# Kernel tuning notes

Measured on AMD Instinct MI355X. Metric: run time of the kernel, lower is better.

The kernel has to match this reference:

```python
import jax, jax.numpy as jnp
import numpy as np

B, WIN, D, H, O, P = 512, 128, 256, 512, 64, 64  # batch, window, input_size, hidden, output, plength


def setup_inputs() -> dict:
    key = jax.random.key(0)
    ks = jax.random.split(key, 14)
    s = 0.05
    return {
        "x": jax.random.normal(ks[0], (B, WIN, D), jnp.float32),
        # AdditiveScore params: V (v_d,), W (v_d, 2H), U (v_d, k_d) with v_d = k_d = D
        "V": jax.random.normal(ks[1], (D,), jnp.float32) * s,
        "W": jax.random.normal(ks[2], (D, 2 * H), jnp.float32) * s,
        "U": jax.random.normal(ks[3], (D, D), jnp.float32) * s,
        # LSTM (1 layer, gate order i,f,g,o): input dim D+O
        "W_ih": jax.random.normal(ks[4], (4 * H, D + O), jnp.float32) * s,
        "W_hh": jax.random.normal(ks[5], (4 * H, H), jnp.float32) * s,
        "b_ih": jax.random.normal(ks[6], (4 * H,), jnp.float32) * s,
        "b_hh": jax.random.normal(ks[7], (4 * H,), jnp.float32) * s,
        # dense: hidden -> output
        "Wd": jax.random.normal(ks[8], (O, H), jnp.float32) * s,
        "bd": jax.random.normal(ks[9], (O,), jnp.float32) * s,
        # context_s / context_c: input -> hidden
        "Ws": jax.random.normal(ks[10], (H, D), jnp.float32) * s,
        "bs": jax.random.normal(ks[11], (H,), jnp.float32) * s,
        "Wc": jax.random.normal(ks[12], (H, D), jnp.float32) * s,
        "bc": jax.random.normal(ks[13], (H,), jnp.float32) * s,
    }


def reference(x, V, W, U, W_ih, W_hh, b_ih, b_hh, Wd, bd, Ws, bs, Wc, bc):
    # initial decoder state from last encoder step
    h0 = jnp.tanh(x[:, -1] @ Ws.T + bs)            # (B, H)
    c0 = jax.nn.sigmoid(x[:, -1] @ Wc.T + bc)      # (B, H)
    y0 = jnp.zeros((x.shape[0], bd.shape[0]), x.dtype)
    # U*k is constant across decode steps: precompute once
    Uk = jnp.einsum('vd,bwd->bvw', U, x)

    def step(carry, _):
        h, c, y = carry
        q = jnp.concatenate([h, c], axis=-1)        # (B, 2H)
        Wq = q @ W.T                                # (B, D)
        # e = V^T tanh(Wq + Uk); softmax over window
        score = jnp.einsum('v,bvw->bw', V, jnp.tanh(Wq[:, :, None] + Uk))
        att = jax.nn.softmax(score, axis=-1)
        ctx = jnp.einsum('bw,bwd->bd', att, x)      # (B, D)
        inp = jnp.concatenate([y, ctx], axis=-1)    # (B, O+D)
        gates = inp @ W_ih.T + h @ W_hh.T + b_ih + b_hh
        i_, f_, g_, o_ = jnp.split(gates, 4, axis=-1)
        c_new = jax.nn.sigmoid(f_) * c + jax.nn.sigmoid(i_) * jnp.tanh(g_)
        h_new = jax.nn.sigmoid(o_) * jnp.tanh(c_new)
        y_new = h_new @ Wd.T + bd                   # (B, O)
        return (h_new, c_new, y_new), (y_new, att)

    _, (ys, atts) = jax.lax.scan(step, (h0, c0, y0), None, length=P)
    predict_y = jnp.transpose(ys, (1, 0, 2))        # (B, P, O)
    weight = jnp.transpose(atts, (1, 0, 2))
    return predict_y, weight
```

## Files before the change

### kernel.cpp

```cpp
#include <hip/hip_runtime.h>
#include <hip/hip_bf16.h>

#define B_   512
#define WIN_ 128
#define D_   256
#define H_   512
#define O_   64
#define P_   64
#define K2H  1024
#define KG   832
#define NQY  320

typedef __attribute__((ext_vector_type(8))) short bf16x8;
typedef __attribute__((ext_vector_type(4))) float f32x4;
using bf16 = __hip_bfloat16;

__device__ __forceinline__ float fast_tanh(float x){
    float e = __expf(2.f * x);
    return 1.f - __fdividef(2.f, e + 1.f);
}
__device__ __forceinline__ float fast_sig(float x){
    return __fdividef(1.f, 1.f + __expf(-x));
}
__device__ __forceinline__ float b_lo(unsigned int u){ return __uint_as_float(u << 16); }
__device__ __forceinline__ float b_hi(unsigned int u){ return __uint_as_float(u & 0xffff0000u); }
__device__ __forceinline__ unsigned int pack2(float a, float b){
    unsigned short sa = __builtin_bit_cast(unsigned short, __float2bfloat16(a));
    unsigned short sb = __builtin_bit_cast(unsigned short, __float2bfloat16(b));
    return (unsigned int)sa | ((unsigned int)sb << 16);
}

__global__ void k_prep(const float* __restrict__ x, const float* __restrict__ W,
                       const float* __restrict__ U, const float* __restrict__ W_ih,
                       const float* __restrict__ W_hh, const float* __restrict__ b_ih,
                       const float* __restrict__ b_hh, const float* __restrict__ Wd,
                       const float* __restrict__ Ws, const float* __restrict__ Wc,
                       bf16* __restrict__ x_bf, bf16* __restrict__ Wcomb,
                       bf16* __restrict__ Wqy, bf16* __restrict__ U_bf,
                       bf16* __restrict__ Wsc, float* __restrict__ bsum,
                       bf16* __restrict__ A0)
{
    const long NX  = (long)B_ * WIN_ * D_;
    const long NWC = (long)2048 * KG;
    const long NWQ = (long)NQY * K2H;
    const long NU  = (long)D_ * D_;
    const long NWS = (long)K2H * D_;
    const long NB  = 2048;
    const long NAY = (long)B_ * O_;
    const long total = NX + NWC + NWQ + NU + NWS + NB + NAY;
    for (long i = (long)blockIdx.x * blockDim.x + threadIdx.x; i < total;
         i += (long)gridDim.x * blockDim.x) {
        long j = i;
        if (j < NX) { x_bf[j] = __float2bfloat16(x[j]); continue; }
        j -= NX;
        if (j < NWC) {
            long n = j / KG, k = j % KG;
            float v = (k < 320) ? W_ih[n * 320 + k] : W_hh[n * 512 + (k - 320)];
            Wcomb[j] = __float2bfloat16(v); continue;
        }
        j -= NWC;
        if (j < NWQ) {
            long n = j / K2H, k = j % K2H;
            float v;
            if (n < 256) v = W[n * K2H + k];
            else { long o = n - 256; v = (k < 512) ? Wd[o * 512 + k] : 0.f; }
            Wqy[j] = __float2bfloat16(v); continue;
        }
        j -= NWQ;
        if (j < NU) { U_bf[j] = __float2bfloat16(U[j]); continue; }
        j -= NU;
        if (j < NWS) {
            long n = j / D_, k = j % D_;
            float v = (n < 512) ? Ws[n * D_ + k] : Wc[(n - 512) * D_ + k];
            Wsc[j] = __float2bfloat16(v); continue;
        }
        j -= NWS;
        if (j < NB) { bsum[j] = b_ih[j] + b_hh[j]; continue; }
        j -= NB;
        { long b = j / O_, o = j % O_; A0[b * KG + o] = __float2bfloat16(0.f); }
    }
}

__global__ void __launch_bounds__(256) k_init2(const bf16* __restrict__ x_bf,
                       const bf16* __restrict__ Wsc, const float* __restrict__ bs,
                       const float* __restrict__ bc, bf16* __restrict__ q_buf,
                       bf16* __restrict__ A0, float* __restrict__ c_f32)
{
    int wave = threadIdx.x >> 6, lane = threadIdx.x & 63;
    int m0 = blockIdx.x * 16;
    int n0 = blockIdx.y * 64 + wave * 16;
    int r = lane & 15, ko = (lane >> 4) * 8, rj = (lane >> 4) * 4;
    const short* xp = (const short*)x_bf;
    const short* wp = (const short*)Wsc;
    f32x4 acc = {};
    #pragma unroll
    for (int k0 = 0; k0 < D_; k0 += 32) {
        bf16x8 a  = *(const bf16x8*)(xp + (long)(m0 + r) * (WIN_ * D_) + 127 * D_ + k0 + ko);
        bf16x8 bb = *(const bf16x8*)(wp + (long)(n0 + r) * D_ + k0 + ko);
        acc = __builtin_amdgcn_mfma_f32_16x16x32_bf16(a, bb, acc, 0, 0, 0);
    }
    int n = n0 + r;
    if (n0 < 512) {
        float bias = bs[n];
        #pragma unroll
        for (int j = 0; j < 4; ++j) {
            int b = m0 + rj + j;
            float hv = fast_tanh(acc[j] + bias);
            bf16 hb = __float2bfloat16(hv);
            q_buf[(long)b * K2H + n]    = hb;
            A0[(long)b * KG + 320 + n]  = hb;
        }
    } else {
        float bias = bc[n - 512];
        #pragma unroll
        for (int j = 0; j < 4; ++j) {
            int b = m0 + rj + j;
            float cv = fast_sig(acc[j] + bias);
            q_buf[(long)b * K2H + n]        = __float2bfloat16(cv);
            c_f32[(long)b * H_ + (n - 512)] = cv;
        }
    }
}

__global__ void __launch_bounds__(256) k_uk(const bf16* __restrict__ U_bf,
                    const bf16* __restrict__ x_bf, bf16* __restrict__ Uk)
{
    __shared__ __align__(16) short xs[64][264];
    int b  = blockIdx.y;
    int v0 = (blockIdx.x >> 1) * 64;
    int w0 = (blockIdx.x & 1) * 64;
    {
        const short* xg = (const short*)x_bf + (long)b * (WIN_ * D_) + (long)w0 * D_;
        int row = threadIdx.x >> 2, cc = (threadIdx.x & 3) * 64;
        #pragma unroll
        for (int i = 0; i < 8; ++i)
            *(bf16x8*)(&xs[row][cc + i * 8]) = *(const bf16x8*)(xg + (long)row * D_ + cc + i * 8);
    }
    __syncthreads();
    int lane = threadIdx.x & 63;
    int wave = threadIdx.x >> 6;
    int r  = lane & 15;
    int ko = (lane >> 4) * 8;
    const short* Up = (const short*)U_bf + (long)(v0 + wave * 16 + r) * D_;
    f32x4 acc[4] = {};
    #pragma unroll 2
    for (int k0 = 0; k0 < D_; k0 += 32) {
        bf16x8 a = *(const bf16x8*)(Up + k0 + ko);
        #pragma unroll
        for (int f = 0; f < 4; ++f) {
            bf16x8 bb = *(const bf16x8*)(&xs[f * 16 + r][k0 + ko]);
            acc[f] = __builtin_amdgcn_mfma_f32_16x16x32_bf16(a, bb, acc[f], 0, 0, 0);
        }
    }
    bf16* up = Uk + (long)b * (D_ * WIN_);
    int vbase = v0 + wave * 16 + (lane >> 4) * 4;
    #pragma unroll
    for (int f = 0; f < 4; ++f) {
        int w = w0 + f * 16 + r;
        #pragma unroll
        for (int j = 0; j < 4; ++j)
            up[(long)(vbase + j) * WIN_ + w] = __float2bfloat16(acc[f][j]);
    }
}

__global__ void __launch_bounds__(64) k_wqy(const bf16* __restrict__ q_buf,
                     const bf16* __restrict__ Wqy, const float* __restrict__ bd,
                     float* __restrict__ Wq, float* __restrict__ out_y,
                     bf16* __restrict__ A_buf, int ystep)
{
    int m0 = blockIdx.x * 16;
    int n0 = blockIdx.y * 32;
    int lane = threadIdx.x & 63;
    int r  = lane & 15;
    int ko = (lane >> 4) * 8;
    const short* qp = (const short*)q_buf;
    const short* wp = (const short*)Wqy;
    f32x4 acc[2] = {};
    for (int k0 = 0; k0 < K2H; k0 += 32) {
        bf16x8 a = *(const bf16x8*)(qp + (long)(m0 + r) * K2H + k0 + ko);
        #pragma unroll
        for (int f = 0; f < 2; ++f) {
            bf16x8 bb = *(const bf16x8*)(wp + (long)(n0 + f*16 + r) * K2H + k0 + ko);
            acc[f] = __builtin_amdgcn_mfma_f32_16x16x32_bf16(a, bb, acc[f], 0, 0, 0);
        }
    }
    #pragma unroll
    for (int f = 0; f < 2; ++f) {
        int n = n0 + f * 16 + r;
        #pragma unroll
        for (int j = 0; j < 4; ++j) {
            int b = m0 + (lane >> 4) * 4 + j;
            float val = acc[f][j];
            if (n < 256) {
                Wq[(long)b * D_ + n] = val;
            } else if (ystep >= 0) {
                int o = n - 256;
                val += bd[o];
                out_y[((long)b * P_ + ystep) * O_ + o] = val;
                A_buf[(long)b * KG + o] = __float2bfloat16(val);
            }
        }
    }
}

__global__ void __launch_bounds__(512) k_att(
    const bf16* __restrict__ x_bf, const bf16* __restrict__ Uk,
    const float* __restrict__ Wq, const float* __restrict__ V,
    bf16* __restrict__ A_cur, float* __restrict__ out_w, int s)
{
    __shared__ float v_s[D_];
    __shared__ float wq_s[2][D_];
    __shared__ float part[2][4][WIN_];
    __shared__ float att_s[2][WIN_];
    __shared__ float cpart[2][2][D_];
    __shared__ float redw[2][4];

    const int tid = threadIdx.x;
    const int b0  = blockIdx.x * 2;
    const int tb  = tid >> 8;
    const int t2  = tid & 255;

    if (tid < D_) v_s[tid] = V[tid];
    { int bb = tid >> 8, n = tid & 255; wq_s[bb][n] = Wq[(long)(b0 + bb) * D_ + n]; }
    __syncthreads();

    const int b = b0 + tb;
    {
        int w2 = t2 & 63, vq = t2 >> 6;
        const unsigned int* ukp =
            (const unsigned int*)(Uk + (long)b * (D_ * WIN_) + (long)vq * 64 * WIN_) + w2;
        float sc0 = 0.f, sc1 = 0.f;
        #pragma unroll 8
        for (int i = 0; i < 64; ++i) {
            unsigned int u = ukp[(long)i * 64];
            int v = vq * 64 + i;
            float wqv = wq_s[tb][v], vv = v_s[v];
            sc0 += vv * fast_tanh(wqv + b_lo(u));
            sc1 += vv * fast_tanh(wqv + b_hi(u));
        }
        part[tb][vq][w2 * 2]     = sc0;
        part[tb][vq][w2 * 2 + 1] = sc1;
    }
    __syncthreads();
    float e = 0.f, scw = 0.f;
    if (t2 < WIN_) {
        scw = part[tb][0][t2] + part[tb][1][t2] + part[tb][2][t2] + part[tb][3][t2];
        float m = scw;
        #pragma unroll
        for (int off = 32; off > 0; off >>= 1) m = fmaxf(m, __shfl_xor(m, off));
        if ((tid & 63) == 0) redw[tb][t2 >> 6] = m;
    }
    __syncthreads();
    if (t2 < WIN_) {
        float m = fmaxf(redw[tb][0], redw[tb][1]);
        e = __expf(scw - m);
        float l = e;
        #pragma unroll
        for (int off = 32; off > 0; off >>= 1) l += __shfl_xor(l, off);
        if ((tid & 63) == 0) redw[tb][2 + (t2 >> 6)] = l;
    }
    __syncthreads();
    if (t2 < WIN_) {
        float l = redw[tb][2] + redw[tb][3];
        float a = __fdividef(e, l);
        att_s[tb][t2] = a;
        out_w[((long)b * P_ + s) * WIN_ + t2] = a;
    }
    __syncthreads();
    {
        int d2 = t2 & 127, wh = t2 >> 7;
        const unsigned int* xp =
            (const unsigned int*)(x_bf + (long)b * (WIN_ * D_) + (long)wh * 64 * D_) + d2;
        float c0 = 0.f, c1 = 0.f;
        #pragma unroll 8
        for (int i = 0; i < 64; ++i) {
            unsigned int u = xp[(long)i * 128];
            float a = att_s[tb][wh * 64 + i];
            c0 += a * b_lo(u);
            c1 += a * b_hi(u);
        }
        cpart[tb][wh][d2 * 2]     = c0;
        cpart[tb][wh][d2 * 2 + 1] = c1;
    }
    __syncthreads();
    if (t2 < 128) {
        int d = t2 * 2;
        float f0 = cpart[tb][0][d] + cpart[tb][1][d];
        float f1 = cpart[tb][0][d + 1] + cpart[tb][1][d + 1];
        *(unsigned int*)(A_cur + (long)b * KG + O_ + d) = pack2(f0, f1);
    }
}

__global__ void __launch_bounds__(256) k_gates(const bf16* __restrict__ A_in,
                     const bf16* __restrict__ Wcomb, const float* __restrict__ bsum,
                     float* __restrict__ c_f32, bf16* __restrict__ A_out,
                     bf16* __restrict__ q_buf)
{
    int m0 = blockIdx.x * 64 + (threadIdx.x >> 6) * 16;
    int j0 = blockIdx.y * 16;
    int lane = threadIdx.x & 63;
    int r  = lane & 15;
    int ko = (lane >> 4) * 8;
    const short* ap = (const short*)A_in;
    const short* wp = (const short*)Wcomb;
    f32x4 acc[4] = {};
    long arow = (long)(m0 + r) * KG;
    #pragma unroll 2
    for (int k0 = 0; k0 < KG; k0 += 32) {
        bf16x8 a = *(const bf16x8*)(ap + arow + k0 + ko);
        #pragma unroll
        for (int g = 0; g < 4; ++g) {
            bf16x8 bb = *(const bf16x8*)(wp + (long)(g * H_ + j0 + r) * KG + k0 + ko);
            acc[g] = __builtin_amdgcn_mfma_f32_16x16x32_bf16(a, bb, acc[g], 0, 0, 0);
        }
    }
    int jj = j0 + r;
    float bi = bsum[jj], bff = bsum[H_ + jj], bg = bsum[2*H_ + jj], bo = bsum[3*H_ + jj];
    int rj = (lane >> 4) * 4;
    #pragma unroll
    for (int j = 0; j < 4; ++j) {
        int b = m0 + rj + j;
        float iv = acc[0][j] + bi;
        float fv = acc[1][j] + bff;
        float gv = acc[2][j] + bg;
        float ov = acc[3][j] + bo;
        float c_old = c_f32[(long)b * H_ + jj];
        float cn = fast_sig(fv) * c_old + fast_sig(iv) * fast_tanh(gv);
        float hn = fast_sig(ov) * fast_tanh(cn);
        c_f32[(long)b * H_ + jj] = cn;
        bf16 hb = __float2bfloat16(hn);
        A_out[(long)b * KG + 320 + jj]  = hb;
        q_buf[(long)b * K2H + jj]       = hb;
        q_buf[(long)b * K2H + H_ + jj]  = __float2bfloat16(cn);
    }
}

__global__ void __launch_bounds__(256) k_yfin(const bf16* __restrict__ q_buf,
                     const bf16* __restrict__ Wqy, const float* __restrict__ bd,
                     float* __restrict__ out_y)
{
    int b = blockIdx.x * 4 + (threadIdx.x >> 6);
    int o = threadIdx.x & 63;
    const short* wdr = (const short*)Wqy + (long)(256 + o) * K2H;
    const short* qh  = (const short*)q_buf + (long)b * K2H;
    float acc = bd[o];
    #pragma unroll 4
    for (int k = 0; k < 512; k += 8) {
        bf16x8 w8 = *(const bf16x8*)(wdr + k);
        bf16x8 h8 = *(const bf16x8*)(qh + k);
        #pragma unroll
        for (int i = 0; i < 8; ++i)
            acc = fmaf(__uint_as_float(((unsigned int)(unsigned short)w8[i]) << 16),
                       __uint_as_float(((unsigned int)(unsigned short)h8[i]) << 16), acc);
    }
    out_y[((long)b * P_ + 63) * O_ + o] = acc;
}

extern "C" void kernel_launch(void* const* d_in, const int* in_sizes, int n_in,
                              void* d_out, int out_size, void* d_ws, size_t ws_size,
                              hipStream_t stream)
{
    const float* x    = (const float*)d_in[0];
    const float* V    = (const float*)d_in[1];
    const float* W    = (const float*)d_in[2];
    const float* U    = (const float*)d_in[3];
    const float* W_ih = (const float*)d_in[4];
    const float* W_hh = (const float*)d_in[5];
    const float* b_ih = (const float*)d_in[6];
    const float* b_hh = (const float*)d_in[7];
    const float* Wd   = (const float*)d_in[8];
    const float* bd   = (const float*)d_in[9];
    const float* Ws   = (const float*)d_in[10];
    const float* bs   = (const float*)d_in[11];
    const float* Wc   = (const float*)d_in[12];
    const float* bc   = (const float*)d_in[13];

    float* out_y = (float*)d_out;
    float* out_w = (float*)d_out + (long)B_ * P_ * O_;

    char* p = (char*)d_ws;
    auto alloc = [&](size_t bytes) { char* r = p; p += (bytes + 255) & ~(size_t)255; return r; };
    bf16*  x_bf  = (bf16*) alloc((size_t)B_ * WIN_ * D_ * 2);
    bf16*  Uk    = (bf16*) alloc((size_t)B_ * D_ * WIN_ * 2);
    bf16*  q_buf = (bf16*) alloc((size_t)B_ * K2H * 2);
    bf16*  A0    = (bf16*) alloc((size_t)B_ * KG * 2);
    bf16*  A1    = (bf16*) alloc((size_t)B_ * KG * 2);
    float* Wq    = (float*)alloc((size_t)B_ * D_ * 4);
    float* c_f32 = (float*)alloc((size_t)B_ * H_ * 4);
    bf16*  Wqy   = (bf16*) alloc((size_t)NQY * K2H * 2);
    bf16*  Wcomb = (bf16*) alloc((size_t)2048 * KG * 2);
    bf16*  U_bf  = (bf16*) alloc((size_t)D_ * D_ * 2);
    bf16*  Wsc   = (bf16*) alloc((size_t)K2H * D_ * 2);
    float* bsum  = (float*)alloc((size_t)2048 * 4);
    bf16*  Abuf[2] = { A0, A1 };

    k_prep<<<4096, 256, 0, stream>>>(x, W, U, W_ih, W_hh, b_ih, b_hh, Wd, Ws, Wc,
                                     x_bf, Wcomb, Wqy, U_bf, Wsc, bsum, A0);
    k_init2<<<dim3(32, 16), 256, 0, stream>>>(x_bf, Wsc, bs, bc, q_buf, A0, c_f32);
    k_uk<<<dim3(8, 512), 256, 0, stream>>>(U_bf, x_bf, Uk);

    for (int s = 0; s < P_; ++s) {
        k_wqy<<<dim3(32, 10), 64, 0, stream>>>(q_buf, Wqy, bd, Wq, out_y,
                                               Abuf[s & 1], s - 1);
        k_att<<<256, 512, 0, stream>>>(x_bf, Uk, Wq, V, Abuf[s & 1], out_w, s);
        k_gates<<<dim3(8, 32), 256, 0, stream>>>(Abuf[s & 1], Wcomb, bsum,
                                                 c_f32, Abuf[(s + 1) & 1], q_buf);
    }
    k_yfin<<<128, 256, 0, stream>>>(q_buf, Wqy, bd, out_y);
}
```

Measured before the change: 2.930 ms.

## Fuse Wq/y projection into gates kernel via split-K partial slabs

Removes the separate per-step k_wqy launch. Each gates block already owns a 64-column slice of h and c, so it computes a split-K partial product of that slice with a sliced W/Wd weight and writes the result to a slab buffer. The attention kernel then sums the 8 partial slabs to form Wq and y. The attention kernel also moves from two batch rows per block to one row per 256-thread block, and x conversion in prep is vectorised. This saves one launch and one q_buf round trip per step, at the cost of extra fp32 slab traffic and an 8-way reduction in k_att.

```diff
diff --git a/kernel.cpp b/kernel.cpp
--- a/kernel.cpp
+++ b/kernel.cpp
@@ -9,7 +9,8 @@
 #define P_   64
 #define K2H  1024
 #define KG   832
-#define NQY  320
+#define NG   2048
+#define NSLN 320
 
 typedef __attribute__((ext_vector_type(8))) short bf16x8;
 typedef __attribute__((ext_vector_type(4))) float f32x4;
@@ -24,6 +25,9 @@
 }
 __device__ __forceinline__ float b_lo(unsigned int u){ return __uint_as_float(u << 16); }
 __device__ __forceinline__ float b_hi(unsigned int u){ return __uint_as_float(u & 0xffff0000u); }
+__device__ __forceinline__ short f2bs(float v){
+    return (short)__builtin_bit_cast(unsigned short, __float2bfloat16(v));
+}
 __device__ __forceinline__ unsigned int pack2(float a, float b){
     unsigned short sa = __builtin_bit_cast(unsigned short, __float2bfloat16(a));
     unsigned short sb = __builtin_bit_cast(unsigned short, __float2bfloat16(b));
@@ -36,37 +40,46 @@
                        const float* __restrict__ b_hh, const float* __restrict__ Wd,
                        const float* __restrict__ Ws, const float* __restrict__ Wc,
                        bf16* __restrict__ x_bf, bf16* __restrict__ Wcomb,
-                       bf16* __restrict__ Wqy, bf16* __restrict__ U_bf,
-                       bf16* __restrict__ Wsc, float* __restrict__ bsum,
-                       bf16* __restrict__ A0)
-{
-    const long NX  = (long)B_ * WIN_ * D_;
-    const long NWC = (long)2048 * KG;
-    const long NWQ = (long)NQY * K2H;
+                       bf16* __restrict__ Wsl, bf16* __restrict__ U_bf,
+                       bf16* __restrict__ Wsc, float* __restrict__ bsum)
+{
+    const long NXv = (long)B_ * WIN_ * D_ / 8;
+    const long NWC = (long)NG * KG;
+    const long NSL = (long)8 * NSLN * 128;
     const long NU  = (long)D_ * D_;
     const long NWS = (long)K2H * D_;
-    const long NB  = 2048;
-    const long NAY = (long)B_ * O_;
-    const long total = NX + NWC + NWQ + NU + NWS + NB + NAY;
+    const long NB  = NG;
+    const long total = NXv + NWC + NSL + NU + NWS + NB;
     for (long i = (long)blockIdx.x * blockDim.x + threadIdx.x; i < total;
          i += (long)gridDim.x * blockDim.x) {
         long j = i;
-        if (j < NX) { x_bf[j] = __float2bfloat16(x[j]); continue; }
-        j -= NX;
+        if (j < NXv) {
+            const float4* xp = (const float4*)x + j * 2;
+            float4 a = xp[0], b = xp[1];
+            bf16x8 v;
+            v[0] = f2bs(a.x); v[1] = f2bs(a.y); v[2] = f2bs(a.z); v[3] = f2bs(a.w);
+            v[4] = f2bs(b.x); v[5] = f2bs(b.y); v[6] = f2bs(b.z); v[7] = f2bs(b.w);
+            *(bf16x8*)((short*)x_bf + j * 8) = v;
+            continue;
+        }
+        j -= NXv;
         if (j < NWC) {
             long n = j / KG, k = j % KG;
             float v = (k < 320) ? W_ih[n * 320 + k] : W_hh[n * 512 + (k - 320)];
             Wcomb[j] = __float2bfloat16(v); continue;
         }
         j -= NWC;
-        if (j < NWQ) {
-            long n = j / K2H, k = j % K2H;
+        if (j < NSL) {
+            long by = j / (NSLN * 128);
+            long rem = j % (NSLN * 128);
+            long n = rem / 128, k = rem % 128;
             float v;
-            if (n < 256) v = W[n * K2H + k];
-            else { long o = n - 256; v = (k < 512) ? Wd[o * 512 + k] : 0.f; }
-            Wqy[j] = __float2bfloat16(v); continue;
-        }
-        j -= NWQ;
+            if (n < 256) v = (k < 64) ? W[n * K2H + by * 64 + k]
+                                      : W[n * K2H + 512 + by * 64 + (k - 64)];
+            else         v = (k < 64) ? Wd[(n - 256) * H_ + by * 64 + k] : 0.f;
+            Wsl[j] = __float2bfloat16(v); continue;
+        }
+        j -= NSL;
         if (j < NU) { U_bf[j] = __float2bfloat16(U[j]); continue; }
         j -= NU;
         if (j < NWS) {
@@ -75,9 +88,7 @@
             Wsc[j] = __float2bfloat16(v); continue;
         }
         j -= NWS;
-        if (j < NB) { bsum[j] = b_ih[j] + b_hh[j]; continue; }
-        j -= NB;
-        { long b = j / O_, o = j % O_; A0[b * KG + o] = __float2bfloat16(0.f); }
+        bsum[j] = b_ih[j] + b_hh[j];
     }
 }
 
@@ -107,8 +118,8 @@
             int b = m0 + rj + j;
             float hv = fast_tanh(acc[j] + bias);
             bf16 hb = __float2bfloat16(hv);
-            q_buf[(long)b * K2H + n]    = hb;
-            A0[(long)b * KG + 320 + n]  = hb;
+            q_buf[(long)b * K2H + n]   = hb;
+            A0[(long)b * KG + 320 + n] = hb;
         }
     } else {
         float bias = bc[n - 512];
@@ -163,70 +174,73 @@
     }
 }
 
-__global__ void __launch_bounds__(64) k_wqy(const bf16* __restrict__ q_buf,
-                     const bf16* __restrict__ Wqy, const float* __restrict__ bd,
-                     float* __restrict__ Wq, float* __restrict__ out_y,
-                     bf16* __restrict__ A_buf, int ystep)
-{
-    int m0 = blockIdx.x * 16;
-    int n0 = blockIdx.y * 32;
-    int lane = threadIdx.x & 63;
-    int r  = lane & 15;
-    int ko = (lane >> 4) * 8;
+__global__ void __launch_bounds__(256) k_slab0(const bf16* __restrict__ q_buf,
+                     const bf16* __restrict__ Wsl, float* __restrict__ slab)
+{
+    int bx = blockIdx.x, by = blockIdx.y;
+    int wave = threadIdx.x >> 6, lane = threadIdx.x & 63;
+    int r = lane & 15, ko = (lane >> 4) * 8, rj = (lane >> 4) * 4;
+    int m0 = bx * 16;
     const short* qp = (const short*)q_buf;
-    const short* wp = (const short*)Wqy;
-    f32x4 acc[2] = {};
-    for (int k0 = 0; k0 < K2H; k0 += 32) {
-        bf16x8 a = *(const bf16x8*)(qp + (long)(m0 + r) * K2H + k0 + ko);
-        #pragma unroll
-        for (int f = 0; f < 2; ++f) {
-            bf16x8 bb = *(const bf16x8*)(wp + (long)(n0 + f*16 + r) * K2H + k0 + ko);
-            acc[f] = __builtin_amdgcn_mfma_f32_16x16x32_bf16(a, bb, acc[f], 0, 0, 0);
-        }
-    }
-    #pragma unroll
-    for (int f = 0; f < 2; ++f) {
-        int n = n0 + f * 16 + r;
-        #pragma unroll
-        for (int j = 0; j < 4; ++j) {
-            int b = m0 + (lane >> 4) * 4 + j;
-            float val = acc[f][j];
-            if (n < 256) {
-                Wq[(long)b * D_ + n] = val;
-            } else if (ystep >= 0) {
-                int o = n - 256;
-                val += bd[o];
-                out_y[((long)b * P_ + ystep) * O_ + o] = val;
-                A_buf[(long)b * KG + o] = __float2bfloat16(val);
-            }
-        }
-    }
-}
-
-__global__ void __launch_bounds__(512) k_att(
+    const short* wp = (const short*)Wsl + (long)by * NSLN * 128;
+    #pragma unroll
+    for (int i = 0; i < 5; ++i) {
+        int n0 = (wave * 5 + i) * 16;
+        f32x4 acc = {};
+        #pragma unroll
+        for (int k0 = 0; k0 < 128; k0 += 32) {
+            long koff = (k0 < 64) ? (by * 64 + k0) : (512 + by * 64 + (k0 - 64));
+            bf16x8 a  = *(const bf16x8*)(qp + (long)(m0 + r) * K2H + koff + ko);
+            bf16x8 bb = *(const bf16x8*)(wp + (long)(n0 + r) * 128 + k0 + ko);
+            acc = __builtin_amdgcn_mfma_f32_16x16x32_bf16(a, bb, acc, 0, 0, 0);
+        }
+        int n = n0 + r;
+        #pragma unroll
+        for (int j = 0; j < 4; ++j)
+            slab[((long)by * B_ + m0 + rj + j) * NSLN + n] = acc[j];
+    }
+}
+
+__global__ void __launch_bounds__(256) k_att(
     const bf16* __restrict__ x_bf, const bf16* __restrict__ Uk,
-    const float* __restrict__ Wq, const float* __restrict__ V,
-    bf16* __restrict__ A_cur, float* __restrict__ out_w, int s)
+    const float* __restrict__ slab, const float* __restrict__ V,
+    const float* __restrict__ bd, bf16* __restrict__ A_cur,
+    float* __restrict__ out_y, float* __restrict__ out_w, int s)
 {
     __shared__ float v_s[D_];
-    __shared__ float wq_s[2][D_];
-    __shared__ float part[2][4][WIN_];
-    __shared__ float att_s[2][WIN_];
-    __shared__ float cpart[2][2][D_];
-    __shared__ float redw[2][4];
-
-    const int tid = threadIdx.x;
-    const int b0  = blockIdx.x * 2;
-    const int tb  = tid >> 8;
-    const int t2  = tid & 255;
-
-    if (tid < D_) v_s[tid] = V[tid];
-    { int bb = tid >> 8, n = tid & 255; wq_s[bb][n] = Wq[(long)(b0 + bb) * D_ + n]; }
-    __syncthreads();
-
-    const int b = b0 + tb;
+    __shared__ float wq_s[D_];
+    __shared__ float part[4][WIN_];
+    __shared__ float att_s[WIN_];
+    __shared__ float cpart[2][D_];
+    __shared__ float redw[4];
+
+    const int b = blockIdx.x;
+    const int t = threadIdx.x;
+
+    v_s[t] = V[t];
     {
-        int w2 = t2 & 63, vq = t2 >> 6;
+        float wsum = 0.f;
+        #pragma unroll
+        for (int by = 0; by < 8; ++by)
+            wsum += slab[((long)by * B_ + b) * NSLN + t];
+        wq_s[t] = wsum;
+    }
+    if (t < O_) {
+        float yv = bd[t];
+        #pragma unroll
+        for (int by = 0; by < 8; ++by)
+            yv += slab[((long)by * B_ + b) * NSLN + 256 + t];
+        if (s > 0) {
+            out_y[((long)b * P_ + (s - 1)) * O_ + t] = yv;
+            A_cur[(long)b * KG + t] = __float2bfloat16(yv);
+        } else {
+            A_cur[(long)b * KG + t] = __float2bfloat16(0.f);
+        }
+    }
+    __syncthreads();
+
+    {
+        int w2 = t & 63, vq = t >> 6;
         const unsigned int* ukp =
             (const unsigned int*)(Uk + (long)b * (D_ * WIN_) + (long)vq * 64 * WIN_) + w2;
         float sc0 = 0.f, sc1 = 0.f;
@@ -234,73 +248,73 @@
         for (int i = 0; i < 64; ++i) {
             unsigned int u = ukp[(long)i * 64];
             int v = vq * 64 + i;
-            float wqv = wq_s[tb][v], vv = v_s[v];
+            float wqv = wq_s[v], vv = v_s[v];
             sc0 += vv * fast_tanh(wqv + b_lo(u));
             sc1 += vv * fast_tanh(wqv + b_hi(u));
         }
-        part[tb][vq][w2 * 2]     = sc0;
-        part[tb][vq][w2 * 2 + 1] = sc1;
+        part[vq][w2 * 2]     = sc0;
+        part[vq][w2 * 2 + 1] = sc1;
     }
     __syncthreads();
     float e = 0.f, scw = 0.f;
-    if (t2 < WIN_) {
-        scw = part[tb][0][t2] + part[tb][1][t2] + part[tb][2][t2] + part[tb][3][t2];
+    if (t < WIN_) {
+        scw = part[0][t] + part[1][t] + part[2][t] + part[3][t];
         float m = scw;
         #pragma unroll
         for (int off = 32; off > 0; off >>= 1) m = fmaxf(m, __shfl_xor(m, off));
-        if ((tid & 63) == 0) redw[tb][t2 >> 6] = m;
-    }
-    __syncthreads();
-    if (t2 < WIN_) {
-        float m = fmaxf(redw[tb][0], redw[tb][1]);
+        if ((t & 63) == 0) redw[t >> 6] = m;
+    }
+    __syncthreads();
+    if (t < WIN_) {
+        float m = fmaxf(redw[0], redw[1]);
         e = __expf(scw - m);
         float l = e;
         #pragma unroll
         for (int off = 32; off > 0; off >>= 1) l += __shfl_xor(l, off);
-        if ((tid & 63) == 0) redw[tb][2 + (t2 >> 6)] = l;
-    }
-    __syncthreads();
-    if (t2 < WIN_) {
-        float l = redw[tb][2] + redw[tb][3];
-        float a = __fdividef(e, l);
-        att_s[tb][t2] = a;
-        out_w[((long)b * P_ + s) * WIN_ + t2] = a;
+        if ((t & 63) == 0) redw[2 + (t >> 6)] = l;
+    }
+    __syncthreads();
+    if (t < WIN_) {
+        float a = __fdividef(e, redw[2] + redw[3]);
+        att_s[t] = a;
+        out_w[((long)b * P_ + s) * WIN_ + t] = a;
     }
     __syncthreads();
     {
-        int d2 = t2 & 127, wh = t2 >> 7;
+        int d2 = t & 127, wh = t >> 7;
         const unsigned int* xp =
             (const unsigned int*)(x_bf + (long)b * (WIN_ * D_) + (long)wh * 64 * D_) + d2;
         float c0 = 0.f, c1 = 0.f;
         #pragma unroll 8
         for (int i = 0; i < 64; ++i) {
             unsigned int u = xp[(long)i * 128];
-            float a = att_s[tb][wh * 64 + i];
+            float a = att_s[wh * 64 + i];
             c0 += a * b_lo(u);
             c1 += a * b_hi(u);
         }
-        cpart[tb][wh][d2 * 2]     = c0;
-        cpart[tb][wh][d2 * 2 + 1] = c1;
-    }
-    __syncthreads();
-    if (t2 < 128) {
-        int d = t2 * 2;
-        float f0 = cpart[tb][0][d] + cpart[tb][1][d];
-        float f1 = cpart[tb][0][d + 1] + cpart[tb][1][d + 1];
+        cpart[wh][d2 * 2]     = c0;
+        cpart[wh][d2 * 2 + 1] = c1;
+    }
+    __syncthreads();
+    if (t < 128) {
+        int d = t * 2;
+        float f0 = cpart[0][d] + cpart[1][d];
+        float f1 = cpart[0][d + 1] + cpart[1][d + 1];
         *(unsigned int*)(A_cur + (long)b * KG + O_ + d) = pack2(f0, f1);
     }
 }
 
 __global__ void __launch_bounds__(256) k_gates(const bf16* __restrict__ A_in,
-                     const bf16* __restrict__ Wcomb, const float* __restrict__ bsum,
-                     float* __restrict__ c_f32, bf16* __restrict__ A_out,
-                     bf16* __restrict__ q_buf)
-{
-    int m0 = blockIdx.x * 64 + (threadIdx.x >> 6) * 16;
-    int j0 = blockIdx.y * 16;
-    int lane = threadIdx.x & 63;
-    int r  = lane & 15;
-    int ko = (lane >> 4) * 8;
+                     const bf16* __restrict__ Wcomb, const bf16* __restrict__ Wsl,
+                     const float* __restrict__ bsum, float* __restrict__ c_f32,
+                     bf16* __restrict__ A_out, float* __restrict__ slab)
+{
+    __shared__ short lhc[16][136];
+    int bx = blockIdx.x, by = blockIdx.y;
+    int wave = threadIdx.x >> 6, lane = threadIdx.x & 63;
+    int r = lane & 15, ko = (lane >> 4) * 8, rj = (lane >> 4) * 4;
+    int m0 = bx * 16;
+    int jw = by * 64 + wave * 16;
     const short* ap = (const short*)A_in;
     const short* wp = (const short*)Wcomb;
     f32x4 acc[4] = {};
@@ -310,50 +324,57 @@
         bf16x8 a = *(const bf16x8*)(ap + arow + k0 + ko);
         #pragma unroll
         for (int g = 0; g < 4; ++g) {
-            bf16x8 bb = *(const bf16x8*)(wp + (long)(g * H_ + j0 + r) * KG + k0 + ko);
+            bf16x8 bb = *(const bf16x8*)(wp + (long)(g * H_ + jw + r) * KG + k0 + ko);
             acc[g] = __builtin_amdgcn_mfma_f32_16x16x32_bf16(a, bb, acc[g], 0, 0, 0);
         }
     }
-    int jj = j0 + r;
-    float bi = bsum[jj], bff = bsum[H_ + jj], bg = bsum[2*H_ + jj], bo = bsum[3*H_ + jj];
-    int rj = (lane >> 4) * 4;
+    int jj = jw + r;
+    float bi = bsum[jj], bf_ = bsum[H_ + jj], bg = bsum[2*H_ + jj], bo = bsum[3*H_ + jj];
     #pragma unroll
     for (int j = 0; j < 4; ++j) {
         int b = m0 + rj + j;
         float iv = acc[0][j] + bi;
-        float fv = acc[1][j] + bff;
+        float fv = acc[1][j] + bf_;
         float gv = acc[2][j] + bg;
         float ov = acc[3][j] + bo;
         float c_old = c_f32[(long)b * H_ + jj];
         float cn = fast_sig(fv) * c_old + fast_sig(iv) * fast_tanh(gv);
         float hn = fast_sig(ov) * fast_tanh(cn);
         c_f32[(long)b * H_ + jj] = cn;
-        bf16 hb = __float2bfloat16(hn);
-        A_out[(long)b * KG + 320 + jj]  = hb;
-        q_buf[(long)b * K2H + jj]       = hb;
-        q_buf[(long)b * K2H + H_ + jj]  = __float2bfloat16(cn);
-    }
-}
-
-__global__ void __launch_bounds__(256) k_yfin(const bf16* __restrict__ q_buf,
-                     const bf16* __restrict__ Wqy, const float* __restrict__ bd,
-                     float* __restrict__ out_y)
+        short hb = f2bs(hn);
+        A_out[(long)b * KG + 320 + jj] = __builtin_bit_cast(bf16, (unsigned short)hb);
+        lhc[rj + j][wave * 16 + r]      = hb;
+        lhc[rj + j][64 + wave * 16 + r] = f2bs(cn);
+    }
+    __syncthreads();
+    const short* wsl = (const short*)Wsl + (long)by * NSLN * 128;
+    #pragma unroll
+    for (int i = 0; i < 5; ++i) {
+        int n0 = (wave * 5 + i) * 16;
+        f32x4 pac = {};
+        #pragma unroll
+        for (int k0 = 0; k0 < 128; k0 += 32) {
+            bf16x8 a  = *(const bf16x8*)(&lhc[r][k0 + ko]);
+            bf16x8 bb = *(const bf16x8*)(wsl + (long)(n0 + r) * 128 + k0 + ko);
+            pac = __builtin_amdgcn_mfma_f32_16x16x32_bf16(a, bb, pac, 0, 0, 0);
+        }
+        int n = n0 + r;
+        #pragma unroll
+        for (int j = 0; j < 4; ++j)
+            slab[((long)by * B_ + m0 + rj + j) * NSLN + n] = pac[j];
+    }
+}
+
+__global__ void __launch_bounds__(256) k_yfin(const float* __restrict__ slab,
+                     const float* __restrict__ bd, float* __restrict__ out_y)
 {
     int b = blockIdx.x * 4 + (threadIdx.x >> 6);
     int o = threadIdx.x & 63;
-    const short* wdr = (const short*)Wqy + (long)(256 + o) * K2H;
-    const short* qh  = (const short*)q_buf + (long)b * K2H;
-    float acc = bd[o];
-    #pragma unroll 4
-    for (int k = 0; k < 512; k += 8) {
-        bf16x8 w8 = *(const bf16x8*)(wdr + k);
-        bf16x8 h8 = *(const bf16x8*)(qh + k);
-        #pragma unroll
-        for (int i = 0; i < 8; ++i)
-            acc = fmaf(__uint_as_float(((unsigned int)(unsigned short)w8[i]) << 16),
-                       __uint_as_float(((unsigned int)(unsigned short)h8[i]) << 16), acc);
-    }
-    out_y[((long)b * P_ + 63) * O_ + o] = acc;
+    float yv = bd[o];
+    #pragma unroll
+    for (int by = 0; by < 8; ++by)
+        yv += slab[((long)by * B_ + b) * NSLN + 256 + o];
+    out_y[((long)b * P_ + 63) * O_ + o] = yv;
 }
 
 extern "C" void kernel_launch(void* const* d_in, const int* in_sizes, int n_in,
@@ -385,26 +406,26 @@
     bf16*  q_buf = (bf16*) alloc((size_t)B_ * K2H * 2);
     bf16*  A0    = (bf16*) alloc((size_t)B_ * KG * 2);
     bf16*  A1    = (bf16*) alloc((size_t)B_ * KG * 2);
-    float* Wq    = (float*)alloc((size_t)B_ * D_ * 4);
     float* c_f32 = (float*)alloc((size_t)B_ * H_ * 4);
-    bf16*  Wqy   = (bf16*) alloc((size_t)NQY * K2H * 2);
-    bf16*  Wcomb = (bf16*) alloc((size_t)2048 * KG * 2);
+    float* slab  = (float*)alloc((size_t)8 * B_ * NSLN * 4);
+    bf16*  Wcomb = (bf16*) alloc((size_t)NG * KG * 2);
+    bf16*  Wsl   = (bf16*) alloc((size_t)8 * NSLN * 128 * 2);
     bf16*  U_bf  = (bf16*) alloc((size_t)D_ * D_ * 2);
     bf16*  Wsc   = (bf16*) alloc((size_t)K2H * D_ * 2);
-    float* bsum  = (float*)alloc((size_t)2048 * 4);
+    float* bsum  = (float*)alloc((size_t)NG * 4);
     bf16*  Abuf[2] = { A0, A1 };
 
     k_prep<<<4096, 256, 0, stream>>>(x, W, U, W_ih, W_hh, b_ih, b_hh, Wd, Ws, Wc,
-                                     x_bf, Wcomb, Wqy, U_bf, Wsc, bsum, A0);
+                                     x_bf, Wcomb, Wsl, U_bf, Wsc, bsum);
     k_init2<<<dim3(32, 16), 256, 0, stream>>>(x_bf, Wsc, bs, bc, q_buf, A0, c_f32);
     k_uk<<<dim3(8, 512), 256, 0, stream>>>(U_bf, x_bf, Uk);
+    k_slab0<<<dim3(32, 8), 256, 0, stream>>>(q_buf, Wsl, slab);
 
     for (int s = 0; s < P_; ++s) {
-        k_wqy<<<dim3(32, 10), 64, 0, stream>>>(q_buf, Wqy, bd, Wq, out_y,
-                                               Abuf[s & 1], s - 1);
-        k_att<<<256, 512, 0, stream>>>(x_bf, Uk, Wq, V, Abuf[s & 1], out_w, s);
-        k_gates<<<dim3(8, 32), 256, 0, stream>>>(Abuf[s & 1], Wcomb, bsum,
-                                                 c_f32, Abuf[(s + 1) & 1], q_buf);
-    }
-    k_yfin<<<128, 256, 0, stream>>>(q_buf, Wqy, bd, out_y);
-}
+        k_att<<<512, 256, 0, stream>>>(x_bf, Uk, slab, V, bd,
+                                       Abuf[s & 1], out_y, out_w, s);
+        k_gates<<<dim3(32, 8), 256, 0, stream>>>(Abuf[s & 1], Wcomb, Wsl, bsum,
+                                                 c_f32, Abuf[(s + 1) & 1], slab);
+    }
+    k_yfin<<<128, 256, 0, stream>>>(slab, bd, out_y);
+}
```

New measurement: 2.509 ms. -14.4%, faster.
